# Kernel optimization log

Hardware: AMD Instinct MI355X
Metric: run time of the kernel (lower is better)

The kernel has to match this reference:

```python
import jax, jax.numpy as jnp
import numpy as np

N, V = 2048, 32000


def setup_inputs() -> dict:
    key = jax.random.key(0)
    k1, k2 = jax.random.split(key)
    logits = jax.random.normal(k1, (N, V), jnp.float32) * 4.0
    # pre-drawn Gumbel noise => categorical sample via argmax(logits + gumbel)
    u = jax.random.uniform(k2, (N, V), jnp.float32, minval=1e-6, maxval=1.0 - 1e-6)
    gumbel = -jnp.log(-jnp.log(u))
    return {
        "logits": logits,
        "gumbel": gumbel,
        "temperature": jnp.float32(0.7),
        "top_p": jnp.float32(0.95),
        "top_k": 50,
        "accept_threshold": jnp.float32(0.9),
    }


def reference(logits, gumbel, temperature, top_p, top_k, accept_threshold):
    neg_inf = jnp.finfo(logits.dtype).min
    x = logits / temperature  # temperature > 0 path

    # --- top_p_logits: sort desc, cumsum of softmax, shift-by-one keep-top mask ---
    order = jnp.argsort(-x, axis=-1)                       # [N, V] descending order
    sorted_x = jnp.take_along_axis(x, order, axis=-1)
    cum = jnp.cumsum(jax.nn.softmax(sorted_x, axis=-1), axis=-1)
    remove_sorted = cum > top_p
    # shift right by one, always keep top-1 token
    remove_sorted = jnp.concatenate(
        [jnp.zeros_like(remove_sorted[..., :1]), remove_sorted[..., :-1]], axis=-1)
    inv = jnp.argsort(order, axis=-1)                      # inverse permutation
    remove = jnp.take_along_axis(remove_sorted, inv, axis=-1)
    x = jnp.where(remove, neg_inf, x)

    # --- top_k_logits: mask everything below the k-th largest ---
    kth = jax.lax.top_k(x, top_k)[0][..., -1:]             # [N, 1]
    x = jnp.where(x < kth, neg_inf, x)

    # --- softmax + categorical sample (Gumbel-argmax) + confidence ---
    probs = jax.nn.softmax(x, axis=-1)                     # [N, V]
    x0 = jnp.argmax(x + gumbel, axis=-1)                   # [N] sampled tokens
    initial_confidence = jnp.take_along_axis(probs, x0[:, None], axis=-1)[:, 0]
    confidence = initial_confidence                        # default (no margin/neg_entropy)

    # --- accept loop: accept above threshold; if none, accept top-1 confidence ---
    high = initial_confidence > accept_threshold           # [N] bool
    any_high = jnp.any(high)
    fallback = jnp.zeros_like(high).at[jnp.argmax(confidence)].set(True)
    accepted = jnp.where(any_high, high, fallback)

    return confidence, x0, initial_confidence, accepted
```

## Files before the change

kernel.cpp:

```cpp
#include <hip/hip_runtime.h>
#include <math.h>
#include <float.h>

#define VOCAB    32000
#define NT       256
#define NWAVES   (NT / 64)
#define CAP      1024
#define KMAX     64
#define KREF     24.0f
#define THETA0   14.0f
#define LOG2E    1.4426950408889634f
#define THT      ((THETA0 - KREF) * LOG2E)
#define FBDELTA  (12.0f * LOG2E)
#define NCHUNK   (VOCAB / 4)

typedef float vf4 __attribute__((ext_vector_type(4)));

__global__ __launch_bounds__(NT) void dream_row_kernel(
    const float* __restrict__ logits,
    const float* __restrict__ gumbel,
    const float* __restrict__ tempP,
    const float* __restrict__ toppP,
    const int*   __restrict__ topkP,
    float* __restrict__ out_conf,
    float* __restrict__ out_x0,
    float* __restrict__ out_iconf)
{
    const int row = blockIdx.x;
    const int tid = threadIdx.x;
    const int lane = tid & 63;
    const int wid  = tid >> 6;
    const size_t base = (size_t)row * VOCAB;
    const vf4* l4 = (const vf4*)(logits + base);
    const float T = tempP[0];
    const float a = (1.0f / T) * LOG2E;
    const float b = -(KREF * LOG2E);

    __shared__ float s_val[CAP];
    __shared__ int   s_idx[CAP];
    __shared__ int   s_cnt;
    __shared__ float wsum[NWAVES], wmax[NWAVES];
    __shared__ float sh_S, sh_m;
    __shared__ float so_val[KMAX];
    __shared__ int   so_idx[KMAX];
    __shared__ int   sh_nk;
    __shared__ float sh_skept;

    if (tid == 0) s_cnt = 0;
    __syncthreads();

    float sA = 0.0f, sB = 0.0f;
    float tmax = -FLT_MAX;
    #pragma unroll 8
    for (int j = tid; j < NCHUNK; j += NT) {
        vf4 v = __builtin_nontemporal_load(&l4[j]);
        float t0 = fmaf(v.x, a, b);
        float t1 = fmaf(v.y, a, b);
        float t2 = fmaf(v.z, a, b);
        float t3 = fmaf(v.w, a, b);
        sA += exp2f(t0);
        sB += exp2f(t1);
        sA += exp2f(t2);
        sB += exp2f(t3);
        tmax = fmaxf(tmax, fmaxf(fmaxf(t0, t1), fmaxf(t2, t3)));
        int bi = j * 4;
        if (t0 > THT) { int p = atomicAdd(&s_cnt, 1); if (p < CAP) { s_val[p] = v.x / T; s_idx[p] = bi;     } }
        if (t1 > THT) { int p = atomicAdd(&s_cnt, 1); if (p < CAP) { s_val[p] = v.y / T; s_idx[p] = bi + 1; } }
        if (t2 > THT) { int p = atomicAdd(&s_cnt, 1); if (p < CAP) { s_val[p] = v.z / T; s_idx[p] = bi + 2; } }
        if (t3 > THT) { int p = atomicAdd(&s_cnt, 1); if (p < CAP) { s_val[p] = v.w / T; s_idx[p] = bi + 3; } }
    }

    float s = sA + sB;
    float mx = tmax;
    #pragma unroll
    for (int o = 32; o > 0; o >>= 1) {
        s  += __shfl_down(s, o, 64);
        mx  = fmaxf(mx, __shfl_down(mx, o, 64));
    }
    if (lane == 0) { wsum[wid] = s; wmax[wid] = mx; }
    __syncthreads();
    if (tid == 0) {
        float St = 0.0f, Mt = -FLT_MAX;
        #pragma unroll
        for (int w = 0; w < NWAVES; ++w) { St += wsum[w]; Mt = fmaxf(Mt, wmax[w]); }
        sh_S = St; sh_m = Mt;
    }
    __syncthreads();
    const float S_K = sh_S;
    const float m_t = sh_m;
    int C = min(s_cnt, CAP);

    if (C < KMAX) {
        if (tid == 0) s_cnt = 0;
        __syncthreads();
        const float th2t = m_t - FBDELTA;
        for (int j = tid; j < NCHUNK; j += NT) {
            vf4 v = __builtin_nontemporal_load(&l4[j]);
            float t0 = fmaf(v.x, a, b);
            float t1 = fmaf(v.y, a, b);
            float t2 = fmaf(v.z, a, b);
            float t3 = fmaf(v.w, a, b);
            int bi = j * 4;
            if (t0 > th2t) { int p = atomicAdd(&s_cnt, 1); if (p < CAP) { s_val[p] = v.x / T; s_idx[p] = bi;     } }
            if (t1 > th2t) { int p = atomicAdd(&s_cnt, 1); if (p < CAP) { s_val[p] = v.y / T; s_idx[p] = bi + 1; } }
            if (t2 > th2t) { int p = atomicAdd(&s_cnt, 1); if (p < CAP) { s_val[p] = v.z / T; s_idx[p] = bi + 2; } }
            if (t3 > th2t) { int p = atomicAdd(&s_cnt, 1); if (p < CAP) { s_val[p] = v.w / T; s_idx[p] = bi + 3; } }
        }
        __syncthreads();
        C = min(s_cnt, CAP);
    }

    for (int c = tid; c < C; c += NT) {
        float vc = s_val[c]; int ic = s_idx[c];
        int r = 0;
        #pragma unroll 4
        for (int j = 0; j < C; ++j) {
            float vj = s_val[j];
            if (vj > vc || (vj == vc && s_idx[j] < ic)) r++;
        }
        if (r < KMAX) { so_val[r] = vc; so_idx[r] = ic; }
    }
    __syncthreads();

    if (tid == 0) {
        int k = topkP[0]; if (k > KMAX) k = KMAX; if (k < 1) k = 1;
        const float topp = toppP[0];
        const int lim = min(C, k);
        float cum = 0.0f;
        float skept = 0.0f;
        int nk = 0;
        for (int j = 0; j < lim; ++j) {
            if (cum > topp) break;
            float e = exp2f(fmaf(so_val[j], LOG2E, b));
            cum += e / S_K;
            skept += e;
            nk++;
        }
        sh_nk = nk;
        sh_skept = skept;
    }
    __syncthreads();
    const int nk = sh_nk;
    const float skept = sh_skept;

    if (wid == 0) {
        float bv = -FLT_MAX; int bi = 0x7FFFFFFF; float bx = 0.0f;
        if (lane < nk) {
            int gi = so_idx[lane];
            bx = so_val[lane];
            bv = bx + gumbel[base + gi];
            bi = gi;
        }
        #pragma unroll
        for (int o = 32; o > 0; o >>= 1) {
            float ov = __shfl_down(bv, o, 64);
            int   oi = __shfl_down(bi, o, 64);
            float ox = __shfl_down(bx, o, 64);
            if (ov > bv || (ov == bv && oi < bi)) { bv = ov; bi = oi; bx = ox; }
        }
        if (lane == 0) {
            float eb = exp2f(fmaf(bx, LOG2E, b));
            float confv = eb / skept;
            out_conf[row]  = confv;
            out_x0[row]    = (float)bi;
            out_iconf[row] = confv;
        }
    }
}

__global__ __launch_bounds__(NT) void accept_kernel(
    const float* __restrict__ conf,
    const float* __restrict__ thrP,
    float* __restrict__ acc_out,
    int N)
{
    __shared__ float rv[NT];
    __shared__ int   ri[NT];
    __shared__ int   ra[NT];
    const int tid = threadIdx.x;
    const float thr = thrP[0];

    float bv = -FLT_MAX; int bi = 0x7FFFFFFF; int any = 0;
    for (int i = tid; i < N; i += NT) {
        float v = conf[i];
        if (v > thr) any = 1;
        if (v > bv) { bv = v; bi = i; }
    }
    rv[tid] = bv; ri[tid] = bi; ra[tid] = any;
    __syncthreads();
    #pragma unroll
    for (int s = NT / 2; s > 0; s >>= 1) {
        if (tid < s) {
            float ov = rv[tid + s]; int oi = ri[tid + s];
            if (ov > rv[tid] || (ov == rv[tid] && oi < ri[tid])) {
                rv[tid] = ov; ri[tid] = oi;
            }
            ra[tid] |= ra[tid + s];
        }
        __syncthreads();
    }
    const int anyHigh = ra[0];
    const int amax = ri[0];
    for (int i = tid; i < N; i += NT) {
        float a;
        if (anyHigh) a = (conf[i] > thr) ? 1.0f : 0.0f;
        else         a = (i == amax) ? 1.0f : 0.0f;
        acc_out[i] = a;
    }
}

extern "C" void kernel_launch(void* const* d_in, const int* in_sizes, int n_in,
                              void* d_out, int out_size, void* d_ws, size_t ws_size,
                              hipStream_t stream)
{
    const float* logits = (const float*)d_in[0];
    const float* gumbel = (const float*)d_in[1];
    const float* tempP  = (const float*)d_in[2];
    const float* toppP  = (const float*)d_in[3];
    const int*   topkP  = (const int*)d_in[4];
    const float* thrP   = (const float*)d_in[5];
    float* out = (float*)d_out;
    const int N = in_sizes[0] / VOCAB;

    dream_row_kernel<<<N, NT, 0, stream>>>(
        logits, gumbel, tempP, toppP, topkP,
        out , out + N , out + 2 * N );

    accept_kernel<<<1, NT, 0, stream>>>(
        out, thrP, out + 3 * N , N);
}
```

Baseline: 530.0 us.

## Stream logits through LDS with async global_load_lds prefetch pipeline

Replaces the direct vectorized global loads in the main row scan with a per-wave, depth-4 ring of asynchronous global-to-LDS loads, using explicit vmcnt waits and sched barriers to overlap memory latency with the exp/max/threshold work. It also adds an occupancy hint to launch bounds and switches the fallback rescan to regular (non-nontemporal) loads. The cost is extra LDS capacity and traffic and hand-tuned waitcnt ordering, which could limit occupancy or serialize on the LDS atomics sharing lgkmcnt.

```diff
diff --git a/kernel.cpp b/kernel.cpp
--- a/kernel.cpp
+++ b/kernel.cpp
@@ -13,10 +13,45 @@
 #define THT      ((THETA0 - KREF) * LOG2E)
 #define FBDELTA  (12.0f * LOG2E)
 #define NCHUNK   (VOCAB / 4)
+#define DEPTH    4
 
 typedef float vf4 __attribute__((ext_vector_type(4)));
-
-__global__ __launch_bounds__(NT) void dream_row_kernel(
+typedef const __attribute__((address_space(1))) void g1v;
+typedef __attribute__((address_space(3))) void l3v;
+
+
+#define PROCESS(v, jj)                                                              \
+    {                                                                               \
+        float t0 = fmaf((v).x, a, b);                                               \
+        float t1 = fmaf((v).y, a, b);                                               \
+        float t2 = fmaf((v).z, a, b);                                               \
+        float t3 = fmaf((v).w, a, b);                                               \
+        sA += exp2f(t0);                                                            \
+        sB += exp2f(t1);                                                            \
+        sA += exp2f(t2);                                                            \
+        sB += exp2f(t3);                                                            \
+        tmax = fmaxf(tmax, fmaxf(fmaxf(t0, t1), fmaxf(t2, t3)));                    \
+        int bi = (jj) * 4;                                                          \
+        if (t0 > THT) { int p = atomicAdd(&s_cnt, 1); if (p < CAP) { s_val[p] = (v).x / T; s_idx[p] = bi;     } } \
+        if (t1 > THT) { int p = atomicAdd(&s_cnt, 1); if (p < CAP) { s_val[p] = (v).y / T; s_idx[p] = bi + 1; } } \
+        if (t2 > THT) { int p = atomicAdd(&s_cnt, 1); if (p < CAP) { s_val[p] = (v).z / T; s_idx[p] = bi + 2; } } \
+        if (t3 > THT) { int p = atomicAdd(&s_cnt, 1); if (p < CAP) { s_val[p] = (v).w / T; s_idx[p] = bi + 3; } } \
+    }
+
+#define ISSUE(k)                                                                    \
+    {                                                                               \
+        const float* gp = logits + base + 4u * ((size_t)(wid + 4 * (k)) * 64 + lane); \
+        __builtin_amdgcn_global_load_lds((g1v*)gp,                                  \
+            (l3v*)&stage[(wid << 10) + (((k) & 3) << 8)], 16, 0, 0);                \
+    }
+
+#define CONSUME(i)                                                                  \
+    {                                                                               \
+        vf4 v = *(const vf4*)&stage[(wid << 10) + (((i) & 3) << 8) + (lane << 2)];  \
+        PROCESS(v, (wid + 4 * (i)) * 64 + lane);                                    \
+    }
+
+__global__ __launch_bounds__(NT, 6) void dream_row_kernel(
     const float* __restrict__ logits,
     const float* __restrict__ gumbel,
     const float* __restrict__ tempP,
@@ -31,11 +66,11 @@
     const int lane = tid & 63;
     const int wid  = tid >> 6;
     const size_t base = (size_t)row * VOCAB;
-    const vf4* l4 = (const vf4*)(logits + base);
     const float T = tempP[0];
     const float a = (1.0f / T) * LOG2E;
     const float b = -(KREF * LOG2E);
 
+    __shared__ float stage[NT * DEPTH * 4];
     __shared__ float s_val[CAP];
     __shared__ int   s_idx[CAP];
     __shared__ int   s_cnt;
@@ -51,24 +86,23 @@
 
     float sA = 0.0f, sB = 0.0f;
     float tmax = -FLT_MAX;
-    #pragma unroll 8
-    for (int j = tid; j < NCHUNK; j += NT) {
-        vf4 v = __builtin_nontemporal_load(&l4[j]);
-        float t0 = fmaf(v.x, a, b);
-        float t1 = fmaf(v.y, a, b);
-        float t2 = fmaf(v.z, a, b);
-        float t3 = fmaf(v.w, a, b);
-        sA += exp2f(t0);
-        sB += exp2f(t1);
-        sA += exp2f(t2);
-        sB += exp2f(t3);
-        tmax = fmaxf(tmax, fmaxf(fmaxf(t0, t1), fmaxf(t2, t3)));
-        int bi = j * 4;
-        if (t0 > THT) { int p = atomicAdd(&s_cnt, 1); if (p < CAP) { s_val[p] = v.x / T; s_idx[p] = bi;     } }
-        if (t1 > THT) { int p = atomicAdd(&s_cnt, 1); if (p < CAP) { s_val[p] = v.y / T; s_idx[p] = bi + 1; } }
-        if (t2 > THT) { int p = atomicAdd(&s_cnt, 1); if (p < CAP) { s_val[p] = v.z / T; s_idx[p] = bi + 2; } }
-        if (t3 > THT) { int p = atomicAdd(&s_cnt, 1); if (p < CAP) { s_val[p] = v.w / T; s_idx[p] = bi + 3; } }
-    }
+    const int nq = (wid == 0) ? 32 : 31;
+
+    asm volatile("s_waitcnt vmcnt(0)" ::: "memory");
+    ISSUE(0); ISSUE(1); ISSUE(2); ISSUE(3);
+
+    for (int i = 0; i + 4 < nq; ++i) {
+        asm volatile("s_waitcnt vmcnt(3)" ::: "memory");
+        __builtin_amdgcn_sched_barrier(0);
+        CONSUME(i);
+        asm volatile("s_waitcnt lgkmcnt(0)" ::: "memory");
+        __builtin_amdgcn_sched_barrier(0);
+        ISSUE(i + 4);
+    }
+    asm volatile("s_waitcnt vmcnt(3)" ::: "memory"); __builtin_amdgcn_sched_barrier(0); CONSUME(nq - 4);
+    asm volatile("s_waitcnt vmcnt(2)" ::: "memory"); __builtin_amdgcn_sched_barrier(0); CONSUME(nq - 3);
+    asm volatile("s_waitcnt vmcnt(1)" ::: "memory"); __builtin_amdgcn_sched_barrier(0); CONSUME(nq - 2);
+    asm volatile("s_waitcnt vmcnt(0)" ::: "memory"); __builtin_amdgcn_sched_barrier(0); CONSUME(nq - 1);
 
     float s = sA + sB;
     float mx = tmax;
@@ -94,8 +128,9 @@
         if (tid == 0) s_cnt = 0;
         __syncthreads();
         const float th2t = m_t - FBDELTA;
+        const vf4* l4 = (const vf4*)(logits + base);
         for (int j = tid; j < NCHUNK; j += NT) {
-            vf4 v = __builtin_nontemporal_load(&l4[j]);
+            vf4 v = l4[j];
             float t0 = fmaf(v.x, a, b);
             float t1 = fmaf(v.y, a, b);
             float t2 = fmaf(v.z, a, b);
```

Result: slower. 547.0 us (+3.2%).

## Process four rows per 1024-thread block with a contiguous cross-row sweep

Applied to the files above, without the earlier changes.

Each block of 1024 threads now handles four rows. The logits are read as one contiguous stream of 256-float chunks covering all four rows, and per-row sums, maxima and candidate lists are kept separately. Candidate selection, top-p/top-k and the Gumbel argmax then run serially for each row inside the block. The aim is longer contiguous loads with more loads in flight per wave, plus fewer blocks. In exchange, the per-row tail work is serialized within a block, there are extra barriers, and register pressure rises.

```diff
diff --git a/kernel.cpp b/kernel.cpp
--- a/kernel.cpp
+++ b/kernel.cpp
@@ -3,20 +3,45 @@
 #include <float.h>
 
 #define VOCAB    32000
-#define NT       256
+#define NT       1024
 #define NWAVES   (NT / 64)
-#define CAP      1024
+#define ACC_NT   256
+#define RPB      4
+#define CPR      125
+#define NCHUNK   8000
+#define CAPG     512
+#define CAPF     1024
 #define KMAX     64
 #define KREF     24.0f
 #define THETA0   14.0f
 #define LOG2E    1.4426950408889634f
 #define THT      ((THETA0 - KREF) * LOG2E)
 #define FBDELTA  (12.0f * LOG2E)
-#define NCHUNK   (VOCAB / 4)
 
 typedef float vf4 __attribute__((ext_vector_type(4)));
 
-__global__ __launch_bounds__(NT) void dream_row_kernel(
+
+#define PROCESS_R(v, c)                                                             \
+    {                                                                               \
+        const int rl = (c) / CPR;                                                   \
+        float t0 = fmaf((v).x, a, b);                                               \
+        float t1 = fmaf((v).y, a, b);                                               \
+        float t2 = fmaf((v).z, a, b);                                               \
+        float t3 = fmaf((v).w, a, b);                                               \
+        float e0 = exp2f(t0), e1 = exp2f(t1), e2 = exp2f(t2), e3 = exp2f(t3);       \
+        float tmc = fmaxf(fmaxf(t0, t1), fmaxf(t2, t3));                            \
+        if (rl == 0)      { sA0 += e0; sB0 += e1; sA0 += e2; sB0 += e3; tm0 = fmaxf(tm0, tmc); } \
+        else if (rl == 1) { sA1 += e0; sB1 += e1; sA1 += e2; sB1 += e3; tm1 = fmaxf(tm1, tmc); } \
+        else if (rl == 2) { sA2 += e0; sB2 += e1; sA2 += e2; sB2 += e3; tm2 = fmaxf(tm2, tmc); } \
+        else              { sA3 += e0; sB3 += e1; sA3 += e2; sB3 += e3; tm3 = fmaxf(tm3, tmc); } \
+        const int bi = ((c) - rl * CPR) * 256 + (lane << 2);                        \
+        if (t0 > THT) { int p = atomicAdd(&s_cnt[rl], 1); if (p < CAPG) { s_val[rl*CAPG+p] = (v).x / T; s_idx[rl*CAPG+p] = bi;     } } \
+        if (t1 > THT) { int p = atomicAdd(&s_cnt[rl], 1); if (p < CAPG) { s_val[rl*CAPG+p] = (v).y / T; s_idx[rl*CAPG+p] = bi + 1; } } \
+        if (t2 > THT) { int p = atomicAdd(&s_cnt[rl], 1); if (p < CAPG) { s_val[rl*CAPG+p] = (v).z / T; s_idx[rl*CAPG+p] = bi + 2; } } \
+        if (t3 > THT) { int p = atomicAdd(&s_cnt[rl], 1); if (p < CAPG) { s_val[rl*CAPG+p] = (v).w / T; s_idx[rl*CAPG+p] = bi + 3; } } \
+    }
+
+__global__ __launch_bounds__(NT, 8) void dream_sweep4_kernel(
     const float* __restrict__ logits,
     const float* __restrict__ gumbel,
     const float* __restrict__ tempP,
@@ -24,164 +49,202 @@
     const int*   __restrict__ topkP,
     float* __restrict__ out_conf,
     float* __restrict__ out_x0,
-    float* __restrict__ out_iconf)
+    float* __restrict__ out_iconf,
+    int nRows)
 {
-    const int row = blockIdx.x;
-    const int tid = threadIdx.x;
+    const int tid  = threadIdx.x;
     const int lane = tid & 63;
     const int wid  = tid >> 6;
-    const size_t base = (size_t)row * VOCAB;
-    const vf4* l4 = (const vf4*)(logits + base);
-    const float T = tempP[0];
-    const float a = (1.0f / T) * LOG2E;
-    const float b = -(KREF * LOG2E);
-
-    __shared__ float s_val[CAP];
-    __shared__ int   s_idx[CAP];
-    __shared__ int   s_cnt;
-    __shared__ float wsum[NWAVES], wmax[NWAVES];
-    __shared__ float sh_S, sh_m;
+    const int r0   = blockIdx.x * RPB;
+    const int nr   = min(RPB, nRows - r0);
+    const int nc   = nr * CPR;
+    const vf4* l4  = (const vf4*)logits + (size_t)r0 * NCHUNK;
+    const float T  = tempP[0];
+    const float a  = (1.0f / T) * LOG2E;
+    const float b  = -(KREF * LOG2E);
+
+    __shared__ float s_val[RPB * CAPG];
+    __shared__ int   s_idx[RPB * CAPG];
+    __shared__ int   s_cnt[RPB];
+    __shared__ float fb_val[CAPF];
+    __shared__ int   fb_idx[CAPF];
+    __shared__ int   fb_cnt;
+    __shared__ float wsum[RPB * NWAVES], wmax[RPB * NWAVES];
+    __shared__ float sh_S[RPB], sh_m[RPB];
     __shared__ float so_val[KMAX];
     __shared__ int   so_idx[KMAX];
     __shared__ int   sh_nk;
     __shared__ float sh_skept;
 
-    if (tid == 0) s_cnt = 0;
-    __syncthreads();
-
-    float sA = 0.0f, sB = 0.0f;
-    float tmax = -FLT_MAX;
-    #pragma unroll 8
-    for (int j = tid; j < NCHUNK; j += NT) {
-        vf4 v = __builtin_nontemporal_load(&l4[j]);
-        float t0 = fmaf(v.x, a, b);
-        float t1 = fmaf(v.y, a, b);
-        float t2 = fmaf(v.z, a, b);
-        float t3 = fmaf(v.w, a, b);
-        sA += exp2f(t0);
-        sB += exp2f(t1);
-        sA += exp2f(t2);
-        sB += exp2f(t3);
-        tmax = fmaxf(tmax, fmaxf(fmaxf(t0, t1), fmaxf(t2, t3)));
-        int bi = j * 4;
-        if (t0 > THT) { int p = atomicAdd(&s_cnt, 1); if (p < CAP) { s_val[p] = v.x / T; s_idx[p] = bi;     } }
-        if (t1 > THT) { int p = atomicAdd(&s_cnt, 1); if (p < CAP) { s_val[p] = v.y / T; s_idx[p] = bi + 1; } }
-        if (t2 > THT) { int p = atomicAdd(&s_cnt, 1); if (p < CAP) { s_val[p] = v.z / T; s_idx[p] = bi + 2; } }
-        if (t3 > THT) { int p = atomicAdd(&s_cnt, 1); if (p < CAP) { s_val[p] = v.w / T; s_idx[p] = bi + 3; } }
-    }
-
-    float s = sA + sB;
-    float mx = tmax;
+    if (tid < RPB) s_cnt[tid] = 0;
+    __syncthreads();
+
+    float sA0 = 0, sB0 = 0, sA1 = 0, sB1 = 0, sA2 = 0, sB2 = 0, sA3 = 0, sB3 = 0;
+    float tm0 = -FLT_MAX, tm1 = -FLT_MAX, tm2 = -FLT_MAX, tm3 = -FLT_MAX;
+
+    int c = wid;
+    for (; c + 112 < nc; c += 128) {
+        vf4 g0 = __builtin_nontemporal_load(&l4[(size_t)(c       ) * 64 + lane]);
+        vf4 g1 = __builtin_nontemporal_load(&l4[(size_t)(c +  16 ) * 64 + lane]);
+        vf4 g2 = __builtin_nontemporal_load(&l4[(size_t)(c +  32 ) * 64 + lane]);
+        vf4 g3 = __builtin_nontemporal_load(&l4[(size_t)(c +  48 ) * 64 + lane]);
+        vf4 g4 = __builtin_nontemporal_load(&l4[(size_t)(c +  64 ) * 64 + lane]);
+        vf4 g5 = __builtin_nontemporal_load(&l4[(size_t)(c +  80 ) * 64 + lane]);
+        vf4 g6 = __builtin_nontemporal_load(&l4[(size_t)(c +  96 ) * 64 + lane]);
+        vf4 g7 = __builtin_nontemporal_load(&l4[(size_t)(c + 112 ) * 64 + lane]);
+        PROCESS_R(g0, c);
+        PROCESS_R(g1, c + 16);
+        PROCESS_R(g2, c + 32);
+        PROCESS_R(g3, c + 48);
+        PROCESS_R(g4, c + 64);
+        PROCESS_R(g5, c + 80);
+        PROCESS_R(g6, c + 96);
+        PROCESS_R(g7, c + 112);
+    }
+    for (; c + 48 < nc; c += 64) {
+        vf4 g0 = __builtin_nontemporal_load(&l4[(size_t)(c      ) * 64 + lane]);
+        vf4 g1 = __builtin_nontemporal_load(&l4[(size_t)(c + 16 ) * 64 + lane]);
+        vf4 g2 = __builtin_nontemporal_load(&l4[(size_t)(c + 32 ) * 64 + lane]);
+        vf4 g3 = __builtin_nontemporal_load(&l4[(size_t)(c + 48 ) * 64 + lane]);
+        PROCESS_R(g0, c);
+        PROCESS_R(g1, c + 16);
+        PROCESS_R(g2, c + 32);
+        PROCESS_R(g3, c + 48);
+    }
+    for (; c < nc; c += 16) {
+        vf4 g0 = __builtin_nontemporal_load(&l4[(size_t)c * 64 + lane]);
+        PROCESS_R(g0, c);
+    }
+
+    float s0 = sA0 + sB0, s1 = sA1 + sB1, s2 = sA2 + sB2, s3 = sA3 + sB3;
     #pragma unroll
     for (int o = 32; o > 0; o >>= 1) {
-        s  += __shfl_down(s, o, 64);
-        mx  = fmaxf(mx, __shfl_down(mx, o, 64));
-    }
-    if (lane == 0) { wsum[wid] = s; wmax[wid] = mx; }
-    __syncthreads();
-    if (tid == 0) {
-        float St = 0.0f, Mt = -FLT_MAX;
+        s0 += __shfl_down(s0, o, 64); tm0 = fmaxf(tm0, __shfl_down(tm0, o, 64));
+        s1 += __shfl_down(s1, o, 64); tm1 = fmaxf(tm1, __shfl_down(tm1, o, 64));
+        s2 += __shfl_down(s2, o, 64); tm2 = fmaxf(tm2, __shfl_down(tm2, o, 64));
+        s3 += __shfl_down(s3, o, 64); tm3 = fmaxf(tm3, __shfl_down(tm3, o, 64));
+    }
+    if (lane == 0) {
+        wsum[0 * NWAVES + wid] = s0; wmax[0 * NWAVES + wid] = tm0;
+        wsum[1 * NWAVES + wid] = s1; wmax[1 * NWAVES + wid] = tm1;
+        wsum[2 * NWAVES + wid] = s2; wmax[2 * NWAVES + wid] = tm2;
+        wsum[3 * NWAVES + wid] = s3; wmax[3 * NWAVES + wid] = tm3;
+    }
+    __syncthreads();
+    if (tid < RPB) {
+        float S = 0.0f, M = -FLT_MAX;
         #pragma unroll
-        for (int w = 0; w < NWAVES; ++w) { St += wsum[w]; Mt = fmaxf(Mt, wmax[w]); }
-        sh_S = St; sh_m = Mt;
-    }
-    __syncthreads();
-    const float S_K = sh_S;
-    const float m_t = sh_m;
-    int C = min(s_cnt, CAP);
-
-    if (C < KMAX) {
-        if (tid == 0) s_cnt = 0;
-        __syncthreads();
-        const float th2t = m_t - FBDELTA;
-        for (int j = tid; j < NCHUNK; j += NT) {
-            vf4 v = __builtin_nontemporal_load(&l4[j]);
-            float t0 = fmaf(v.x, a, b);
-            float t1 = fmaf(v.y, a, b);
-            float t2 = fmaf(v.z, a, b);
-            float t3 = fmaf(v.w, a, b);
-            int bi = j * 4;
-            if (t0 > th2t) { int p = atomicAdd(&s_cnt, 1); if (p < CAP) { s_val[p] = v.x / T; s_idx[p] = bi;     } }
-            if (t1 > th2t) { int p = atomicAdd(&s_cnt, 1); if (p < CAP) { s_val[p] = v.y / T; s_idx[p] = bi + 1; } }
-            if (t2 > th2t) { int p = atomicAdd(&s_cnt, 1); if (p < CAP) { s_val[p] = v.z / T; s_idx[p] = bi + 2; } }
-            if (t3 > th2t) { int p = atomicAdd(&s_cnt, 1); if (p < CAP) { s_val[p] = v.w / T; s_idx[p] = bi + 3; } }
-        }
-        __syncthreads();
-        C = min(s_cnt, CAP);
-    }
-
-    for (int c = tid; c < C; c += NT) {
-        float vc = s_val[c]; int ic = s_idx[c];
-        int r = 0;
-        #pragma unroll 4
-        for (int j = 0; j < C; ++j) {
-            float vj = s_val[j];
-            if (vj > vc || (vj == vc && s_idx[j] < ic)) r++;
-        }
-        if (r < KMAX) { so_val[r] = vc; so_idx[r] = ic; }
-    }
-    __syncthreads();
-
-    if (tid == 0) {
-        int k = topkP[0]; if (k > KMAX) k = KMAX; if (k < 1) k = 1;
-        const float topp = toppP[0];
-        const int lim = min(C, k);
-        float cum = 0.0f;
-        float skept = 0.0f;
-        int nk = 0;
-        for (int j = 0; j < lim; ++j) {
-            if (cum > topp) break;
-            float e = exp2f(fmaf(so_val[j], LOG2E, b));
-            cum += e / S_K;
-            skept += e;
-            nk++;
-        }
-        sh_nk = nk;
-        sh_skept = skept;
-    }
-    __syncthreads();
-    const int nk = sh_nk;
-    const float skept = sh_skept;
-
-    if (wid == 0) {
-        float bv = -FLT_MAX; int bi = 0x7FFFFFFF; float bx = 0.0f;
-        if (lane < nk) {
-            int gi = so_idx[lane];
-            bx = so_val[lane];
-            bv = bx + gumbel[base + gi];
-            bi = gi;
-        }
-        #pragma unroll
-        for (int o = 32; o > 0; o >>= 1) {
-            float ov = __shfl_down(bv, o, 64);
-            int   oi = __shfl_down(bi, o, 64);
-            float ox = __shfl_down(bx, o, 64);
-            if (ov > bv || (ov == bv && oi < bi)) { bv = ov; bi = oi; bx = ox; }
-        }
-        if (lane == 0) {
-            float eb = exp2f(fmaf(bx, LOG2E, b));
-            float confv = eb / skept;
-            out_conf[row]  = confv;
-            out_x0[row]    = (float)bi;
-            out_iconf[row] = confv;
-        }
+        for (int w = 0; w < NWAVES; ++w) {
+            S += wsum[tid * NWAVES + w];
+            M = fmaxf(M, wmax[tid * NWAVES + w]);
+        }
+        sh_S[tid] = S; sh_m[tid] = M;
+    }
+    __syncthreads();
+
+    for (int r = 0; r < nr; ++r) {
+        const size_t base = (size_t)(r0 + r) * VOCAB;
+        int C = min(s_cnt[r], CAPG);
+        const float* rv = &s_val[r * CAPG];
+        const int*   ri = &s_idx[r * CAPG];
+
+        if (C < KMAX) {
+            if (tid == 0) fb_cnt = 0;
+            __syncthreads();
+            const float th2t = sh_m[r] - FBDELTA;
+            const vf4* lr = (const vf4*)(logits + base);
+            for (int j = tid; j < NCHUNK; j += NT) {
+                vf4 v = __builtin_nontemporal_load(&lr[j]);
+                float t0 = fmaf(v.x, a, b);
+                float t1 = fmaf(v.y, a, b);
+                float t2 = fmaf(v.z, a, b);
+                float t3 = fmaf(v.w, a, b);
+                int bi = j * 4;
+                if (t0 > th2t) { int p = atomicAdd(&fb_cnt, 1); if (p < CAPF) { fb_val[p] = v.x / T; fb_idx[p] = bi;     } }
+                if (t1 > th2t) { int p = atomicAdd(&fb_cnt, 1); if (p < CAPF) { fb_val[p] = v.y / T; fb_idx[p] = bi + 1; } }
+                if (t2 > th2t) { int p = atomicAdd(&fb_cnt, 1); if (p < CAPF) { fb_val[p] = v.z / T; fb_idx[p] = bi + 2; } }
+                if (t3 > th2t) { int p = atomicAdd(&fb_cnt, 1); if (p < CAPF) { fb_val[p] = v.w / T; fb_idx[p] = bi + 3; } }
+            }
+            __syncthreads();
+            C = min(fb_cnt, CAPF);
+            rv = fb_val; ri = fb_idx;
+        }
+
+        for (int cc = tid; cc < C; cc += NT) {
+            float vc = rv[cc]; int ic = ri[cc];
+            int rk = 0;
+            #pragma unroll 4
+            for (int j = 0; j < C; ++j) {
+                float vj = rv[j];
+                if (vj > vc || (vj == vc && ri[j] < ic)) rk++;
+            }
+            if (rk < KMAX) { so_val[rk] = vc; so_idx[rk] = ic; }
+        }
+        __syncthreads();
+
+        if (tid == 0) {
+            int k = topkP[0]; if (k > KMAX) k = KMAX; if (k < 1) k = 1;
+            const float topp = toppP[0];
+            const int lim = min(C, k);
+            float cum = 0.0f;
+            float skept = 0.0f;
+            int nk = 0;
+            for (int j = 0; j < lim; ++j) {
+                if (cum > topp) break;
+                float e = exp2f(fmaf(so_val[j], LOG2E, b));
+                cum += e / sh_S[r];
+                skept += e;
+                nk++;
+            }
+            sh_nk = nk;
+            sh_skept = skept;
+        }
+        __syncthreads();
+        const int nk = sh_nk;
+        const float skept = sh_skept;
+
+        if (wid == 0) {
+            float bv = -FLT_MAX; int bi = 0x7FFFFFFF; float bx = 0.0f;
+            if (lane < nk) {
+                int gi = so_idx[lane];
+                bx = rv == fb_val ? so_val[lane] : so_val[lane];
+                bx = so_val[lane];
+                bv = bx + gumbel[base + gi];
+                bi = gi;
+            }
+            #pragma unroll
+            for (int o = 32; o > 0; o >>= 1) {
+                float ov = __shfl_down(bv, o, 64);
+                int   oi = __shfl_down(bi, o, 64);
+                float ox = __shfl_down(bx, o, 64);
+                if (ov > bv || (ov == bv && oi < bi)) { bv = ov; bi = oi; bx = ox; }
+            }
+            if (lane == 0) {
+                float eb = exp2f(fmaf(bx, LOG2E, b));
+                float confv = eb / skept;
+                out_conf[r0 + r]  = confv;
+                out_x0[r0 + r]    = (float)bi;
+                out_iconf[r0 + r] = confv;
+            }
+        }
+        __syncthreads();
     }
 }
 
-__global__ __launch_bounds__(NT) void accept_kernel(
+__global__ __launch_bounds__(ACC_NT) void accept_kernel(
     const float* __restrict__ conf,
     const float* __restrict__ thrP,
     float* __restrict__ acc_out,
     int N)
 {
-    __shared__ float rv[NT];
-    __shared__ int   ri[NT];
-    __shared__ int   ra[NT];
+    __shared__ float rv[ACC_NT];
+    __shared__ int   ri[ACC_NT];
+    __shared__ int   ra[ACC_NT];
     const int tid = threadIdx.x;
     const float thr = thrP[0];
 
     float bv = -FLT_MAX; int bi = 0x7FFFFFFF; int any = 0;
-    for (int i = tid; i < N; i += NT) {
+    for (int i = tid; i < N; i += ACC_NT) {
         float v = conf[i];
         if (v > thr) any = 1;
         if (v > bv) { bv = v; bi = i; }
@@ -189,7 +252,7 @@
     rv[tid] = bv; ri[tid] = bi; ra[tid] = any;
     __syncthreads();
     #pragma unroll
-    for (int s = NT / 2; s > 0; s >>= 1) {
+    for (int s = ACC_NT / 2; s > 0; s >>= 1) {
         if (tid < s) {
             float ov = rv[tid + s]; int oi = ri[tid + s];
             if (ov > rv[tid] || (ov == rv[tid] && oi < ri[tid])) {
@@ -201,7 +264,7 @@
     }
     const int anyHigh = ra[0];
     const int amax = ri[0];
-    for (int i = tid; i < N; i += NT) {
+    for (int i = tid; i < N; i += ACC_NT) {
         float a;
         if (anyHigh) a = (conf[i] > thr) ? 1.0f : 0.0f;
         else         a = (i == amax) ? 1.0f : 0.0f;
@@ -221,11 +284,12 @@
     const float* thrP   = (const float*)d_in[5];
     float* out = (float*)d_out;
     const int N = in_sizes[0] / VOCAB;
-
-    dream_row_kernel<<<N, NT, 0, stream>>>(
+    const int nBlocks = (N + RPB - 1) / RPB;
+
+    dream_sweep4_kernel<<<nBlocks, NT, 0, stream>>>(
         logits, gumbel, tempP, toppP, topkP,
-        out , out + N , out + 2 * N );
-
-    accept_kernel<<<1, NT, 0, stream>>>(
+        out , out + N , out + 2 * N , N);
+
+    accept_kernel<<<1, ACC_NT, 0, stream>>>(
         out, thrP, out + 3 * N , N);
 }
```

Measured after the change: 582.8 us. 10.0% more time.
